# Optimization experiments

Measured on AMD Instinct MI355X. Metric: run time of the kernel, lower is better.

The kernel has to match this reference:

```python
import jax, jax.numpy as jnp
import numpy as np

B, T, D = 2, 4096, 1024
H, HD = 16, 64
KV = H * HD  # 1024


def setup_inputs() -> dict:
    key = jax.random.key(0)
    ks = jax.random.split(key, 6)
    sc = lambda k, shape, s: jax.random.normal(k, shape, jnp.float32) * s
    return {
        "x": sc(ks[0], (B, T, D), 1.0),
        "W_in": sc(ks[1], (D, 4 * KV), D ** -0.5),      # in_proj (in, out) layout
        "W_ba": sc(ks[2], (D, 2 * H), D ** -0.5),       # ba_proj
        "conv_w": sc(ks[3], (3 * KV, 1, 4), 0.5),       # depthwise conv, (O, I/groups=1, K)
        "dt_bias": jnp.ones((H,), jnp.float32),
        "A_log": jnp.log(jax.random.uniform(ks[4], (H,), jnp.float32, 1e-3, 16.0)),
        "norm_w": jnp.ones((HD,), jnp.float32),
        "W_o": sc(ks[5], (KV, D), KV ** -0.5),
    }


def _l2norm(t, eps=1e-6):
    return t * jax.lax.rsqrt(jnp.sum(t * t, axis=-1, keepdims=True) + eps)


def reference(x, W_in, W_ba, conv_w, dt_bias, A_log, norm_w, W_o):
    Bb, Tt, _ = x.shape
    qkvz = x @ W_in                                  # [B,T,4*KV]
    q, k, v, z = jnp.split(qkvz, 4, axis=-1)
    b, a = jnp.split(x @ W_ba, 2, axis=-1)           # [B,T,H] each

    # causal depthwise conv (kernel 4, left pad 3) + SiLU on concat(q,k,v)
    qkv = jnp.concatenate([q, k, v], axis=-1).transpose(0, 2, 1)  # [B,3KV,T]
    qkv = jax.lax.conv_general_dilated(
        qkv, conv_w, window_strides=(1,), padding=[(3, 0)],
        feature_group_count=3 * KV, dimension_numbers=("NCH", "OIH", "NCH"))
    qkv = jax.nn.silu(qkv).transpose(0, 2, 1)        # [B,T,3KV]
    q, k, v = jnp.split(qkv, 3, axis=-1)

    rs = lambda t: t.reshape(Bb, Tt, H, HD)
    q, k, v, z = rs(q), rs(k), rs(v), rs(z)

    beta = jax.nn.sigmoid(b)                         # [B,T,H]
    A = jnp.exp(jnp.maximum(A_log, -2.3))            # [H]
    g = -A * jax.nn.softplus(a + dt_bias)            # [B,T,H], log decay <= 0

    # fla use_qk_l2norm_in_kernel=True: l2-normalize q,k; q scaled by d^-0.5
    q = _l2norm(q) * (HD ** -0.5)
    k = _l2norm(k)

    # gated delta rule recurrence over time (state S: [B,H,dk,dv])
    tm = lambda t: jnp.swapaxes(t, 0, 1)             # time-major

    def step(S, inp):
        qt, kt, vt, gt, bt = inp
        S = S * jnp.exp(gt)[..., None, None]
        pred = jnp.einsum("bhk,bhkv->bhv", kt, S)
        S = S + jnp.einsum("bhk,bhv->bhkv", kt, (vt - pred) * bt[..., None])
        o = jnp.einsum("bhk,bhkv->bhv", qt, S)
        return S, o

    S0 = jnp.zeros((Bb, H, HD, HD), jnp.float32)
    _, y = jax.lax.scan(step, S0, (tm(q), tm(k), tm(v), tm(g), tm(beta)))
    y = jnp.swapaxes(y, 0, 1)                        # [B,T,H,HD]

    # RMSNormGated over head_dim, gated by silu(z)
    y = y * jax.lax.rsqrt(jnp.mean(y * y, axis=-1, keepdims=True) + 1e-6)
    y = (norm_w * y) * jax.nn.silu(z)

    return y.reshape(Bb, Tt, KV) @ W_o
```

## Files before the change

kernel.cpp:

```cpp
#include <hip/hip_runtime.h>

typedef unsigned short u16;
typedef unsigned int u32;
typedef __attribute__((ext_vector_type(8))) __bf16 bf16x8;
typedef __attribute__((ext_vector_type(8))) _Float16 f16x8;
typedef __attribute__((ext_vector_type(4))) _Float16 f16x4;
typedef __attribute__((ext_vector_type(4))) float f32x4;

#define DEV __device__ __forceinline__

DEV u16 f2bf(float f) {
  u32 u = __float_as_uint(f);
  u += 0x7FFFu + ((u >> 16) & 1u);
  return (u16)(u >> 16);
}
DEV float bf2f(u16 h) { return __uint_as_float(((u32)h) << 16); }
DEV void splitbf(float f, u16& hi, u16& lo) {
  u16 h = f2bf(f);
  hi = h;
  lo = f2bf(f - bf2f(h));
}
DEV void split4(float4 v, ushort4& hh, ushort4& ll) {
  splitbf(v.x, hh.x, ll.x);
  splitbf(v.y, hh.y, ll.y);
  splitbf(v.z, hh.z, ll.z);
  splitbf(v.w, hh.w, ll.w);
}
DEV int SW(int r, int c) { return r * 64 + ((c) ^ ((r & 7) << 3)); }

DEV int SWG(int r, int c) {
  int db = ((r & 1) << 2) | ((c >> 3) & 3);
  int dbp = db ^ ((r >> 1) & 7);
  return ((r >> 1) << 6) | (dbp << 3) | (c & 7);
}
DEV size_t gidx_swz(size_t row, int col, int rowlen) {
  int rr7 = (int)((row >> 1) & 7);
  int db = (int)(((row & 1) << 2) | ((col >> 3) & 3));
  int dbp = db ^ rr7;
  size_t rowp = (row & ~(size_t)1) | (size_t)(dbp >> 2);
  int colp = (col & ~31) | ((dbp & 3) << 3) | (col & 7);
  return rowp * (size_t)rowlen + colp;
}

#define MFMA16(a,b,c) __builtin_amdgcn_mfma_f32_16x16x32_bf16((a),(b),(c),0,0,0)
#define MFMAH(a,b,c)  __builtin_amdgcn_mfma_f32_16x16x32_f16((a),(b),(c),0,0,0)
#define GLDS16(g,l) __builtin_amdgcn_global_load_lds((__attribute__((address_space(1))) void*)(g), (__attribute__((address_space(3))) void*)(l), 16, 0, 0)

DEV f32x4 mm3(bf16x8 ah, bf16x8 al, bf16x8 bh, bf16x8 bl, f32x4 acc) {
  acc = MFMA16(ah, bl, acc);
  acc = MFMA16(al, bh, acc);
  acc = MFMA16(ah, bh, acc);
  return acc;
}

__global__ __launch_bounds__(256) void k_cast_h(const float* __restrict__ in, _Float16* __restrict__ out, int n) {
  int idx = (blockIdx.x * 256 + threadIdx.x) * 4;
  if (idx + 3 < n) {
    float4 v = *(const float4*)(in + idx);
    f16x4 o = {(_Float16)v.x, (_Float16)v.y, (_Float16)v.z, (_Float16)v.w};
    const size_t row = (size_t)(idx >> 10);
    const int col = idx & 1023;
    *(f16x4*)(out + gidx_swz(row, col, 1024)) = o;
  }
}

__global__ __launch_bounds__(256) void k_transpose_h(const float* __restrict__ in, _Float16* __restrict__ out, int R, int Cc) {
  __shared__ float tile[64][65];
  int c0 = blockIdx.x * 64, r0 = blockIdx.y * 64;
  int lr = threadIdx.x >> 6, lc = threadIdx.x & 63;
#pragma unroll
  for (int i = 0; i < 16; ++i) {
    int r = lr + i * 4;
    tile[r][lc] = in[(size_t)(r0 + r) * Cc + c0 + lc];
  }
  __syncthreads();
#pragma unroll
  for (int i = 0; i < 16; ++i) {
    int oc = lr + i * 4;
    out[gidx_swz((size_t)(c0 + oc), r0 + lc, R)] = (_Float16)tile[lc][oc];
  }
}

__global__ __launch_bounds__(256) void k_transpose(const float* __restrict__ in, u16* __restrict__ out, int R, int Cc) {
  __shared__ float tile[64][65];
  int c0 = blockIdx.x * 64, r0 = blockIdx.y * 64;
  int lr = threadIdx.x >> 6, lc = threadIdx.x & 63;
#pragma unroll
  for (int i = 0; i < 16; ++i) {
    int r = lr + i * 4;
    tile[r][lc] = in[(size_t)(r0 + r) * Cc + c0 + lc];
  }
  __syncthreads();
#pragma unroll
  for (int i = 0; i < 16; ++i) {
    int oc = lr + i * 4;
    out[gidx_swz((size_t)(c0 + oc), r0 + lc, R)] = f2bf(tile[lc][oc]);
  }
}

__global__ __launch_bounds__(512, 2) void k_gemm_h(const _Float16* __restrict__ A, const _Float16* __restrict__ Bt,
                                                   u16* __restrict__ Cq, u16* __restrict__ Cz, int M, int N, int K) {
  __shared__ __align__(16) u16 As[2][256 * 32];
  __shared__ __align__(16) u16 Bs[2][256 * 32];
  const int tid = threadIdx.x;
  const int nwg = gridDim.x * gridDim.y;
  int bid = blockIdx.y * gridDim.x + blockIdx.x;
  bid = (bid & 7) * (nwg >> 3) + (bid >> 3);
  const int m0 = (bid / gridDim.x) * 256, n0 = (bid % gridDim.x) * 256;
  const int w = tid >> 6, l = tid & 63;
  const int wr = (w >> 1) * 64, wc = (w & 1) * 128;
  const int lrow = l & 15, lk = (l >> 4) * 8, rbase = (l >> 4) * 4;

  f32x4 acc[4][8];
#pragma unroll
  for (int i = 0; i < 4; ++i)
#pragma unroll
    for (int j = 0; j < 8; ++j) acc[i][j] = {0.f, 0.f, 0.f, 0.f};

  const _Float16* aBase = A + (size_t)m0 * K;
  const _Float16* bBase = Bt + (size_t)n0 * K;
  const int srow0 = tid >> 2, scol0 = (tid & 3) * 8;
  const int srow1 = (tid + 512) >> 2;

  auto STAGE = [&](int buf, int k0) {
    GLDS16(aBase + (size_t)srow0 * K + k0 + scol0, &As[buf][tid * 8]);
    GLDS16(aBase + (size_t)srow1 * K + k0 + scol0, &As[buf][4096 + tid * 8]);
    GLDS16(bBase + (size_t)srow0 * K + k0 + scol0, &Bs[buf][tid * 8]);
    GLDS16(bBase + (size_t)srow1 * K + k0 + scol0, &Bs[buf][4096 + tid * 8]);
  };

  STAGE(0, 0);
  __syncthreads();
  int cur = 0;
  for (int k0 = 0; k0 < K; k0 += 32) {
    if (k0 + 32 < K) STAGE(cur ^ 1, k0 + 32);
    f16x8 af[4], bfr[8];
#pragma unroll
    for (int i = 0; i < 4; ++i) af[i] = *(const f16x8*)&As[cur][SWG(wr + i * 16 + lrow, lk)];
#pragma unroll
    for (int j = 0; j < 8; ++j) bfr[j] = *(const f16x8*)&Bs[cur][SWG(wc + j * 16 + lrow, lk)];
#pragma unroll
    for (int i = 0; i < 4; ++i)
#pragma unroll
      for (int j = 0; j < 8; ++j) acc[i][j] = MFMAH(af[i], bfr[j], acc[i][j]);
    __syncthreads();
    cur ^= 1;
  }
#pragma unroll
  for (int i = 0; i < 4; ++i)
#pragma unroll
    for (int j = 0; j < 8; ++j)
#pragma unroll
      for (int r = 0; r < 4; ++r) {
        int row = m0 + wr + i * 16 + rbase + r;
        int col = n0 + wc + j * 16 + lrow;
        if (col < 3072) Cq[(size_t)row * 3072 + col] = f2bf(acc[i][j][r]);
        else            Cz[(size_t)row * 1024 + col - 3072] = f2bf(acc[i][j][r]);
      }
}

__global__ __launch_bounds__(256, 2) void k_gemm2(const u16* __restrict__ Ah, const u16* __restrict__ Al,
                                               const u16* __restrict__ Bt, float* __restrict__ Cf,
                                               int M, int N, int K) {
  __shared__ __align__(16) u16 Ash[2][128 * 32];
  __shared__ __align__(16) u16 Asl[2][128 * 32];
  __shared__ __align__(16) u16 Bs[2][128 * 32];
  const int tid = threadIdx.x;
  const int nwg = gridDim.x * gridDim.y;
  int bid = blockIdx.y * gridDim.x + blockIdx.x;
  bid = (bid & 7) * (nwg >> 3) + (bid >> 3);
  const int m0 = (bid / gridDim.x) * 128, n0 = (bid % gridDim.x) * 128;
  const int w = tid >> 6, l = tid & 63;
  const int wr = (w >> 1) * 64, wc = (w & 1) * 64;
  const int lrow = l & 15, lk = (l >> 4) * 8, rbase = (l >> 4) * 4;
  const int srow = tid >> 2, scol = (tid & 3) * 8;

  f32x4 acc[4][4];
#pragma unroll
  for (int i = 0; i < 4; ++i)
#pragma unroll
    for (int j = 0; j < 4; ++j) acc[i][j] = {0.f, 0.f, 0.f, 0.f};

  const u16* ahBase = Ah + (size_t)m0 * K;
  const u16* alBase = Al + (size_t)m0 * K;
  const u16* bBase  = Bt + (size_t)n0 * K;

  auto STAGE = [&](int buf, int k0) {
    GLDS16(ahBase + (size_t)srow * K + k0 + scol,        &Ash[buf][tid * 8]);
    GLDS16(ahBase + (size_t)(srow + 64) * K + k0 + scol, &Ash[buf][2048 + tid * 8]);
    GLDS16(alBase + (size_t)srow * K + k0 + scol,        &Asl[buf][tid * 8]);
    GLDS16(alBase + (size_t)(srow + 64) * K + k0 + scol, &Asl[buf][2048 + tid * 8]);
    GLDS16(bBase + (size_t)srow * K + k0 + scol,         &Bs[buf][tid * 8]);
    GLDS16(bBase + (size_t)(srow + 64) * K + k0 + scol,  &Bs[buf][2048 + tid * 8]);
  };

  STAGE(0, 0);
  __syncthreads();
  int cur = 0;
  for (int k0 = 0; k0 < K; k0 += 32) {
    if (k0 + 32 < K) STAGE(cur ^ 1, k0 + 32);
    bf16x8 afh[4], afl[4], bfr[4];
#pragma unroll
    for (int i = 0; i < 4; ++i) afh[i] = *(const bf16x8*)&Ash[cur][SWG(wr + i * 16 + lrow, lk)];
#pragma unroll
    for (int i = 0; i < 4; ++i) afl[i] = *(const bf16x8*)&Asl[cur][SWG(wr + i * 16 + lrow, lk)];
#pragma unroll
    for (int j = 0; j < 4; ++j) bfr[j] = *(const bf16x8*)&Bs[cur][SWG(wc + j * 16 + lrow, lk)];
#pragma unroll
    for (int i = 0; i < 4; ++i)
#pragma unroll
      for (int j = 0; j < 4; ++j) {
        acc[i][j] = MFMA16(afl[i], bfr[j], acc[i][j]);
        acc[i][j] = MFMA16(afh[i], bfr[j], acc[i][j]);
      }
    __syncthreads();
    cur ^= 1;
  }
#pragma unroll
  for (int i = 0; i < 4; ++i)
#pragma unroll
    for (int j = 0; j < 4; ++j)
#pragma unroll
      for (int r = 0; r < 4; ++r) {
        int row = m0 + wr + i * 16 + rbase + r;
        int col = n0 + wc + j * 16 + lrow;
        Cf[(size_t)row * N + col] = acc[i][j][r];
      }
}

__global__ __launch_bounds__(256) void k_ba(const float* __restrict__ x, const float* __restrict__ Wba,
                                            const float* __restrict__ dt_bias, const float* __restrict__ A_log,
                                            float* __restrict__ betaO, float* __restrict__ gO) {
  __shared__ float xs[4][1024];
  const int wid = threadIdx.x >> 6, lane = threadIdx.x & 63;
  const int m = blockIdx.x * 4 + wid;
#pragma unroll
  for (int i = 0; i < 16; ++i) xs[wid][lane + 64 * i] = x[(size_t)m * 1024 + lane + 64 * i];
  __syncthreads();
  const int n = lane & 31, half = lane >> 5;
  float acc = 0.f;
  const float* wp = Wba + n;
  const int kk0 = half * 512;
#pragma unroll 8
  for (int kk = kk0; kk < kk0 + 512; ++kk) acc += xs[wid][kk] * wp[kk * 32];
  acc += __shfl_xor(acc, 32);
  if (lane < 32) {
    if (n < 16) {
      betaO[(size_t)m * 16 + n] = 1.f / (1.f + expf(-acc));
    } else {
      int h = n - 16;
      float xx = acc + dt_bias[h];
      float sp = (xx > 20.f) ? xx : log1pf(expf(xx));
      gO[(size_t)m * 16 + h] = -expf(fmaxf(A_log[h], -2.3f)) * sp;
    }
  }
}

__global__ __launch_bounds__(256) void k_conv(const u16* __restrict__ qkv3, const float* __restrict__ convw,
                                              u16* __restrict__ qhG, u16* __restrict__ qlG,
                                              u16* __restrict__ khG, u16* __restrict__ klG,
                                              u16* __restrict__ vhG, u16* __restrict__ vlG) {
  __shared__ float cs[3072];
  __shared__ float innorm[32];
  const int bt = blockIdx.x;
  const int bb = bt >> 12, tt = bt & 4095;
  const int tid = threadIdx.x;
  const size_t rb = (size_t)bb * 4096;
#pragma unroll
  for (int s = 0; s < 3; ++s) {
    const int c4 = tid * 4 + s * 1024;
    float cwa[4][4];
#pragma unroll
    for (int e = 0; e < 4; ++e) {
      float4 t = *(const float4*)&convw[(c4 + e) * 4];
      cwa[e][0] = t.x; cwa[e][1] = t.y; cwa[e][2] = t.z; cwa[e][3] = t.w;
    }
    float acc[4] = {0.f, 0.f, 0.f, 0.f};
#pragma unroll
    for (int j = 0; j < 4; ++j) {
      const int tau = tt - 3 + j;
      if (tau >= 0) {
        ushort4 kv = *(const ushort4*)&qkv3[(rb + tau) * 3072 + c4];
        acc[0] += bf2f(kv.x) * cwa[0][j];
        acc[1] += bf2f(kv.y) * cwa[1][j];
        acc[2] += bf2f(kv.z) * cwa[2][j];
        acc[3] += bf2f(kv.w) * cwa[3][j];
      }
    }
#pragma unroll
    for (int e = 0; e < 4; ++e) cs[c4 + e] = acc[e] / (1.f + expf(-acc[e]));
  }
  __syncthreads();
  {
    const int grp = tid >> 3, off = (tid & 7) * 8;
    const float* p = cs + grp * 64 + off;
    float s = 0.f;
#pragma unroll
    for (int i = 0; i < 8; ++i) s += p[i] * p[i];
    s += __shfl_xor(s, 1); s += __shfl_xor(s, 2); s += __shfl_xor(s, 4);
    if ((tid & 7) == 0) innorm[grp] = rsqrtf(s + 1e-6f);
  }
  __syncthreads();
  const int h = tid >> 4, d4 = (tid & 15) * 4;
  const size_t ob = ((size_t)(bb * 16 + h) * 64 + (tt >> 6)) * 4096 + SW(tt & 63, d4);
  {
    const int ci = h * 64 + d4;
    const float sc = innorm[h] * 0.125f;
    float4 o = {cs[ci] * sc, cs[ci + 1] * sc, cs[ci + 2] * sc, cs[ci + 3] * sc};
    ushort4 hh, ll;
    split4(o, hh, ll);
    *(ushort4*)&qhG[ob] = hh;
    *(ushort4*)&qlG[ob] = ll;
  }
  {
    const int ci = 1024 + h * 64 + d4;
    const float sc = innorm[16 + h];
    float4 o = {cs[ci] * sc, cs[ci + 1] * sc, cs[ci + 2] * sc, cs[ci + 3] * sc};
    ushort4 hh, ll;
    split4(o, hh, ll);
    *(ushort4*)&khG[ob] = hh;
    *(ushort4*)&klG[ob] = ll;
  }
  {
    const int ci = 2048 + h * 64 + d4;
    float4 o = {cs[ci], cs[ci + 1], cs[ci + 2], cs[ci + 3]};
    ushort4 hh, ll;
    split4(o, hh, ll);
    *(ushort4*)&vhG[ob] = hh;
    *(ushort4*)&vlG[ob] = ll;
  }
}

__global__ __launch_bounds__(64) void k_prep(const u16* __restrict__ khG, const u16* __restrict__ klG,
                                             const float* __restrict__ gG, const float* __restrict__ betaG,
                                             float* __restrict__ gcG, u16* __restrict__ Tgh, u16* __restrict__ Tgl) {
  __shared__ __align__(16) char pmem[16384];
  u16* Kbh = (u16*)pmem;
  u16* Kbl = (u16*)(pmem + 8192);
  float* Af = (float*)pmem;
  __shared__ float gcs[64], bs[64];
  const int bhc = blockIdx.x;
  const int c = bhc & 63, h = (bhc >> 6) & 15, bb = bhc >> 10;
  const int lane = threadIdx.x;
  const int t0 = c * 64;
  const size_t rowbase = (size_t)bb * 4096;
  const size_t ktile = (size_t)bhc * 4096;
#pragma unroll
  for (int i = 0; i < 8; ++i) {
    const int idx = lane + 64 * i;
    GLDS16(khG + ktile + idx * 8, &Kbh[idx * 8]);
    GLDS16(klG + ktile + idx * 8, &Kbl[idx * 8]);
  }
  {
    float gv = gG[(rowbase + t0 + lane) * 16 + h];
    float sc = gv;
#pragma unroll
    for (int off = 1; off < 64; off <<= 1) {
      float o = __shfl_up(sc, off);
      if (lane >= off) sc += o;
    }
    gcs[lane] = sc;
    bs[lane] = betaG[(rowbase + t0 + lane) * 16 + h];
    gcG[(size_t)bhc * 64 + lane] = sc;
  }
  __syncthreads();
  const int lrow = lane & 15, lk8 = (lane >> 4) * 8, rbase = (lane >> 4) * 4;
  f32x4 acc[4][4];
#pragma unroll
  for (int i = 0; i < 4; ++i)
#pragma unroll
    for (int j = 0; j < 4; ++j) acc[i][j] = {0.f, 0.f, 0.f, 0.f};
#pragma unroll
  for (int ks = 0; ks < 2; ++ks) {
    bf16x8 afh[4], afl[4], bfh[4], bfl[4];
#pragma unroll
    for (int i = 0; i < 4; ++i) {
      afh[i] = *(const bf16x8*)&Kbh[SW(i * 16 + lrow, ks * 32 + lk8)];
      afl[i] = *(const bf16x8*)&Kbl[SW(i * 16 + lrow, ks * 32 + lk8)];
    }
#pragma unroll
    for (int j = 0; j < 4; ++j) {
      bfh[j] = *(const bf16x8*)&Kbh[SW(j * 16 + lrow, ks * 32 + lk8)];
      bfl[j] = *(const bf16x8*)&Kbl[SW(j * 16 + lrow, ks * 32 + lk8)];
    }
#pragma unroll
    for (int i = 0; i < 4; ++i)
#pragma unroll
      for (int j = 0; j < 4; ++j) acc[i][j] = mm3(afh[i], afl[i], bfh[j], bfl[j], acc[i][j]);
  }
  __syncthreads();
#pragma unroll
  for (int i = 0; i < 4; ++i)
#pragma unroll
    for (int j = 0; j < 4; ++j)
#pragma unroll
      for (int r = 0; r < 4; ++r) {
        int t = i * 16 + rbase + r, s = j * 16 + lrow;
        Af[t * 64 + s] = (s < t) ? bs[t] * expf(gcs[t] - gcs[s]) * acc[i][j][r] : 0.f;
      }
  __syncthreads();
  float x[64];
#pragma unroll
  for (int t = 0; t < 64; ++t) {
    float sum = 0.f;
#pragma unroll
    for (int s4 = 0; s4 + 4 <= t; s4 += 4) {
      float4 a4 = *(const float4*)&Af[t * 64 + s4];
      sum += a4.x * x[s4] + a4.y * x[s4 + 1] + a4.z * x[s4 + 2] + a4.w * x[s4 + 3];
    }
#pragma unroll
    for (int s = (t & ~3); s < t; ++s) sum += Af[t * 64 + s] * x[s];
    x[t] = ((t == lane) ? 1.f : 0.f) - sum;
  }
#pragma unroll
  for (int t = 0; t < 64; ++t) {
    u16 hi, lo;
    splitbf(x[t], hi, lo);
    Tgh[(size_t)bhc * 4096 + SW(t, lane)] = hi;
    Tgl[(size_t)bhc * 4096 + SW(t, lane)] = lo;
  }
}

__global__ __launch_bounds__(256) void k_mn(const u16* __restrict__ khG, const u16* __restrict__ klG,
                                            const u16* __restrict__ vhG, const u16* __restrict__ vlG,
                                            const u16* __restrict__ Tgh, const u16* __restrict__ Tgl,
                                            const float* __restrict__ gcG, const float* __restrict__ betaG,
                                            u16* __restrict__ Mh, u16* __restrict__ Ml,
                                            u16* __restrict__ Nh, u16* __restrict__ Nl) {
  extern __shared__ __align__(16) char smem[];
  u16* base = (u16*)smem;
  u16* Tbh  = base + 0 * 4096;
  u16* Tbl  = base + 1 * 4096;
  u16* X1h  = base + 2 * 4096;
  u16* X1l  = base + 3 * 4096;
  u16* KdTh = base + 4 * 4096;
  u16* KdTl = base + 5 * 4096;
  u16* X2h  = base + 6 * 4096;
  u16* X2l  = base + 7 * 4096;
  float* gcs = (float*)(base + 8 * 4096);
  float* bs  = gcs + 64;

  const int bhc = blockIdx.x;
  const int c = bhc & 63, h = (bhc >> 6) & 15, bb = bhc >> 10;
  const int tid = threadIdx.x, w = tid >> 6, l = tid & 63;
  const int lrow = l & 15, lk8 = (l >> 4) * 8, rbase = (l >> 4) * 4;
  const int t0 = c * 64;
  const size_t rowbase = (size_t)bb * 4096;
  const size_t ktile = (size_t)bhc * 4096;

  if (tid < 64) {
    gcs[tid] = gcG[(size_t)bhc * 64 + tid];
    bs[tid] = betaG[(rowbase + t0 + tid) * 16 + h];
  }
#pragma unroll
  for (int i = 0; i < 2; ++i) {
    const int idx = tid + 256 * i;
    const int off = idx * 8;
    *(float4*)&Tbh[off] = *(const float4*)&Tgh[(size_t)bhc * 4096 + off];
    *(float4*)&Tbl[off] = *(const float4*)&Tgl[(size_t)bhc * 4096 + off];
  }
  __syncthreads();
  const float gc63 = gcs[63];
#pragma unroll
  for (int i = 0; i < 16; ++i) {
    const int flat = tid + 256 * i;
    const int s = flat >> 6, d = flat & 63;
    const int sws = SW(s, d);
    const float kf = bf2f(khG[ktile + sws]) + bf2f(klG[ktile + sws]);
    const float gv = gcs[s], bv = bs[s];
    u16 hh, ll;
    splitbf(bv * expf(gv) * kf, hh, ll);
    X1h[SW(d, s)] = hh; X1l[SW(d, s)] = ll;
    splitbf(expf(gc63 - gv) * kf, hh, ll);
    KdTh[SW(d, s)] = hh; KdTl[SW(d, s)] = ll;
    const float vv = bf2f(vhG[ktile + sws]) + bf2f(vlG[ktile + sws]);
    splitbf(bv * vv, hh, ll);
    X2h[SW(d, s)] = hh; X2l[SW(d, s)] = ll;
  }
  __syncthreads();

  f32x4 aW[4], aU[4];
#pragma unroll
  for (int j = 0; j < 4; ++j) { aW[j] = {0.f,0.f,0.f,0.f}; aU[j] = {0.f,0.f,0.f,0.f}; }
#pragma unroll
  for (int ks = 0; ks < 2; ++ks) {
    const int ao = SW(w * 16 + lrow, ks * 32 + lk8);
    bf16x8 aTh = *(const bf16x8*)&Tbh[ao];
    bf16x8 aTl = *(const bf16x8*)&Tbl[ao];
#pragma unroll
    for (int j = 0; j < 4; ++j) {
      const int bo = SW(j * 16 + lrow, ks * 32 + lk8);
      aW[j] = mm3(aTh, aTl, *(const bf16x8*)&X1h[bo], *(const bf16x8*)&X1l[bo], aW[j]);
      aU[j] = mm3(aTh, aTl, *(const bf16x8*)&X2h[bo], *(const bf16x8*)&X2l[bo], aU[j]);
    }
  }
  __syncthreads();
#pragma unroll
  for (int j = 0; j < 4; ++j)
#pragma unroll
    for (int r = 0; r < 4; ++r) {
      const int t = w * 16 + rbase + r, dcol = j * 16 + lrow;
      u16 hh, ll;
      splitbf(aW[j][r], hh, ll);
      X1h[SW(dcol, t)] = hh; X1l[SW(dcol, t)] = ll;
      splitbf(aU[j][r], hh, ll);
      X2h[SW(dcol, t)] = hh; X2l[SW(dcol, t)] = ll;
    }
  __syncthreads();

  f32x4 aM[4], aN[4];
#pragma unroll
  for (int j = 0; j < 4; ++j) { aM[j] = {0.f,0.f,0.f,0.f}; aN[j] = {0.f,0.f,0.f,0.f}; }
#pragma unroll
  for (int ks = 0; ks < 2; ++ks) {
    const int ao = SW(w * 16 + lrow, ks * 32 + lk8);
    bf16x8 aKh = *(const bf16x8*)&KdTh[ao];
    bf16x8 aKl = *(const bf16x8*)&KdTl[ao];
#pragma unroll
    for (int j = 0; j < 4; ++j) {
      const int bo = SW(j * 16 + lrow, ks * 32 + lk8);
      aM[j] = mm3(aKh, aKl, *(const bf16x8*)&X1h[bo], *(const bf16x8*)&X1l[bo], aM[j]);
      aN[j] = mm3(aKh, aKl, *(const bf16x8*)&X2h[bo], *(const bf16x8*)&X2l[bo], aN[j]);
    }
  }
  __syncthreads();
  const float decC = expf(gc63);
#pragma unroll
  for (int j = 0; j < 4; ++j)
#pragma unroll
    for (int r = 0; r < 4; ++r) {
      const int d = w * 16 + rbase + r, d2 = j * 16 + lrow;
      u16 hh, ll;
      splitbf(((d == d2) ? decC : 0.f) - aM[j][r], hh, ll);
      X1h[SW(d, d2)] = hh; X1l[SW(d, d2)] = ll;
      splitbf(aN[j][r], hh, ll);
      X2h[SW(d, d2)] = hh; X2l[SW(d, d2)] = ll;
    }
  __syncthreads();
#pragma unroll
  for (int i = 0; i < 2; ++i) {
    const int idx = tid + 256 * i;
    const int off = idx * 8;
    *(float4*)&Mh[(size_t)bhc * 4096 + off] = *(const float4*)&X1h[off];
    *(float4*)&Ml[(size_t)bhc * 4096 + off] = *(const float4*)&X1l[off];
    *(float4*)&Nh[(size_t)bhc * 4096 + off] = *(const float4*)&X2h[off];
    *(float4*)&Nl[(size_t)bhc * 4096 + off] = *(const float4*)&X2l[off];
  }
}

__global__ __launch_bounds__(256) void k_seg(const u16* __restrict__ Mh, const u16* __restrict__ Ml,
                                             const u16* __restrict__ Nh, const u16* __restrict__ Nl,
                                             u16* __restrict__ Msegh, u16* __restrict__ Msegl,
                                             u16* __restrict__ Nsegh, u16* __restrict__ Nsegl) {
  extern __shared__ __align__(16) char smem[];
  u16* base = (u16*)smem;
  u16* MaTh = base + 0 * 4096;
  u16* MaTl = base + 1 * 4096;
  u16* NaTh = base + 2 * 4096;
  u16* NaTl = base + 3 * 4096;
  u16* sMh  = base + 4 * 4096;
  u16* sMl  = base + 5 * 4096;
  u16* sNh  = base + 6 * 4096;
  u16* sNl  = base + 7 * 4096;

  const int blk = blockIdx.x;
  const size_t cbase = (size_t)(blk >> 3) * 64 + (blk & 7) * 8;
  const int tid = threadIdx.x, w = tid >> 6, l = tid & 63;
  const int lrow = l & 15, lk8 = (l >> 4) * 8, rbase = (l >> 4) * 4;

#pragma unroll
  for (int i = 0; i < 2; ++i) {
    const int off = (tid + 256 * i) * 8;
    *(float4*)&sMh[off] = *(const float4*)&Mh[cbase * 4096 + off];
    *(float4*)&sMl[off] = *(const float4*)&Ml[cbase * 4096 + off];
    *(float4*)&sNh[off] = *(const float4*)&Nh[cbase * 4096 + off];
    *(float4*)&sNl[off] = *(const float4*)&Nl[cbase * 4096 + off];
  }
  __syncthreads();
#pragma unroll
  for (int i = 0; i < 16; ++i) {
    const int flat = tid + 256 * i;
    const int a = flat >> 6, b = flat & 63;
    MaTh[SW(a, b)] = sMh[SW(b, a)];
    MaTl[SW(a, b)] = sMl[SW(b, a)];
    NaTh[SW(a, b)] = sNh[SW(b, a)];
    NaTl[SW(a, b)] = sNl[SW(b, a)];
  }
  __syncthreads();

  for (int j = 1; j < 8; ++j) {
#pragma unroll
    for (int i = 0; i < 2; ++i) {
      const int off = (tid + 256 * i) * 8;
      *(float4*)&sMh[off] = *(const float4*)&Mh[(cbase + j) * 4096 + off];
      *(float4*)&sMl[off] = *(const float4*)&Ml[(cbase + j) * 4096 + off];
      *(float4*)&sNh[off] = *(const float4*)&Nh[(cbase + j) * 4096 + off];
      *(float4*)&sNl[off] = *(const float4*)&Nl[(cbase + j) * 4096 + off];
    }
    __syncthreads();
    f32x4 aM2[4], aN2[4];
#pragma unroll
    for (int jj = 0; jj < 4; ++jj) { aM2[jj] = {0.f,0.f,0.f,0.f}; aN2[jj] = {0.f,0.f,0.f,0.f}; }
#pragma unroll
    for (int ks = 0; ks < 2; ++ks) {
      const int ao = SW(w * 16 + lrow, ks * 32 + lk8);
      bf16x8 aCh = *(const bf16x8*)&sMh[ao];
      bf16x8 aCl = *(const bf16x8*)&sMl[ao];
#pragma unroll
      for (int jj = 0; jj < 4; ++jj) {
        const int bo = SW(jj * 16 + lrow, ks * 32 + lk8);
        aM2[jj] = mm3(aCh, aCl, *(const bf16x8*)&MaTh[bo], *(const bf16x8*)&MaTl[bo], aM2[jj]);
        aN2[jj] = mm3(aCh, aCl, *(const bf16x8*)&NaTh[bo], *(const bf16x8*)&NaTl[bo], aN2[jj]);
      }
    }
    __syncthreads();
#pragma unroll
    for (int jj = 0; jj < 4; ++jj)
#pragma unroll
      for (int r = 0; r < 4; ++r) {
        const int t = w * 16 + rbase + r, col = jj * 16 + lrow;
        u16 hh, ll;
        splitbf(aM2[jj][r], hh, ll);
        MaTh[SW(col, t)] = hh; MaTl[SW(col, t)] = ll;
        const float nv = aN2[jj][r] + bf2f(sNh[SW(t, col)]) + bf2f(sNl[SW(t, col)]);
        splitbf(nv, hh, ll);
        NaTh[SW(col, t)] = hh; NaTl[SW(col, t)] = ll;
      }
    __syncthreads();
  }
#pragma unroll
// ... 225 lines not shown
      for (int j = 0; j < 2; ++j) {
        const int bo = SW((jh * 2 + j) * 16 + lrow, ks * 32 + lk8);
        au[j] = mm3(aTh, aTl, *(const bf16x8*)&RTh[bo], *(const bf16x8*)&RTl[bo], au[j]);
      }
    }
#pragma unroll
    for (int j = 0; j < 2; ++j)
#pragma unroll
      for (int r = 0; r < 4; ++r) {
        u16 uh, ul;
        splitbf(au[j][r], uh, ul);
        const int o = SW((jh * 2 + j) * 16 + lrow, wrow * 16 + rbase + r);
        UTh[o] = uh;
        UTl[o] = ul;
      }
    __syncthreads();

    if (pf) {
      GLDS16(Tgh + (size_t)(bh * 64 + (c + 1)) * 4096 + o8, &Tbh[o8]);
      GLDS16(Tgl + (size_t)(bh * 64 + (c + 1)) * 4096 + o8, &Tbl[o8]);
    }

    f32x4 amu[2], as_[2];
#pragma unroll
    for (int j = 0; j < 2; ++j) { amu[j] = {0.f,0.f,0.f,0.f}; as_[j] = {0.f,0.f,0.f,0.f}; }
#pragma unroll
    for (int ks = 0; ks < 2; ++ks) {
      const int ao = SW(wrow * 16 + lrow, ks * 32 + lk8);
      bf16x8 aMh = *(const bf16x8*)&Mqh[ao];
      bf16x8 aMl = *(const bf16x8*)&Mql[ao];
      bf16x8 aKdh = *(const bf16x8*)&KdTh[ao];
      bf16x8 aKdl = *(const bf16x8*)&KdTl[ao];
#pragma unroll
      for (int j = 0; j < 2; ++j) {
        const int bo = SW((jh * 2 + j) * 16 + lrow, ks * 32 + lk8);
        bf16x8 bUh = *(const bf16x8*)&UTh[bo];
        bf16x8 bUl = *(const bf16x8*)&UTl[bo];
        amu[j] = mm3(aMh, aMl, bUh, bUl, amu[j]);
        as_[j] = mm3(aKdh, aKdl, bUh, bUl, as_[j]);
      }
    }
    float yv_[4][2];
#pragma unroll
    for (int r = 0; r < 4; ++r) {
      const int t = wrow * 16 + rbase + r;
      const float gt = etF[t];
      float ss = 0.f;
#pragma unroll
      for (int j = 0; j < 2; ++j) {
        yv_[r][j] = gt * aqs[j][r] + amu[j][r];
        ss += yv_[r][j] * yv_[r][j];
      }
      ss += __shfl_xor(ss, 1); ss += __shfl_xor(ss, 2); ss += __shfl_xor(ss, 4); ss += __shfl_xor(ss, 8);
      if (lrow == 0) ssP[jh * 64 + t] = ss;
    }
    __syncthreads();
#pragma unroll
    for (int r = 0; r < 4; ++r) {
      const int t = wrow * 16 + rbase + r;
      const float rstd = rsqrtf((ssP[t] + ssP[64 + t]) * (1.f / 64.f) + 1e-6f);
#pragma unroll
      for (int j = 0; j < 2; ++j) {
        const int col = (jh * 2 + j) * 16 + lrow;
        const float zz = bf2f(Zb[SW(t, col)]);
        const float yv = yv_[r][j] * rstd * nws[col] * (zz / (1.f + expf(-zz)));
        u16 yh, yl;
        splitbf(yv, yh, yl);
        Ybh[SW(t, col)] = yh;
        Ybl[SW(t, col)] = yl;
      }
    }
    {
      const float decC = etF[63];
#pragma unroll
      for (int j = 0; j < 2; ++j)
#pragma unroll
        for (int r = 0; r < 4; ++r) {
          const int d = wrow * 16 + rbase + r, col = (jh * 2 + j) * 16 + lrow;
          const int o = SW(col, d);
          const float s0 = bf2f(SbTh[o]) + bf2f(SbTl[o]);
          const float sv = decC * s0 + as_[j][r];
          u16 sh, sl;
          splitbf(sv, sh, sl);
          SbTh[o] = sh;
          SbTl[o] = sl;
        }
    }
    __syncthreads();

    {
      const size_t gsw = gidx_swz(rowbase + t0 + zr, h * 64 + zc8, 1024);
      *(float4*)&Yhi[gsw] = *(const float4*)&Ybh[SW(zr, zc8)];
      *(float4*)&Ylo[gsw] = *(const float4*)&Ybl[SW(zr, zc8)];
    }
    if (pf) {
      *(float4*)&Zb[SW(zr, zc8)] = pz;
      if (tid < 64) {
        float g63 = __shfl(pgc, 63);
        gcs[tid] = pgc; bs[tid] = pbs;
        esF[tid] = expf(g63 - pgc);
        etF[tid] = expf(pgc);
      }
    }
    __syncthreads();
  }
}

extern "C" void kernel_launch(void* const* d_in, const int* in_sizes, int n_in,
                              void* d_out, int out_size, void* d_ws, size_t ws_size,
                              hipStream_t stream) {
  (void)in_sizes; (void)n_in; (void)out_size; (void)ws_size;
  const float* x       = (const float*)d_in[0];
  const float* W_in    = (const float*)d_in[1];
  const float* W_ba    = (const float*)d_in[2];
  const float* conv_w  = (const float*)d_in[3];
  const float* dt_bias = (const float*)d_in[4];
  const float* A_log   = (const float*)d_in[5];
  const float* norm_w  = (const float*)d_in[6];
  const float* W_o     = (const float*)d_in[7];
  float* out = (float*)d_out;
  char* ws = (char*)d_ws;
  const size_t MB = 1048576;

  _Float16* xh = (_Float16*)(ws + 0);
  u16* MhB   = (u16*)(ws + 0);
  u16* YhiB  = (u16*)(ws + 0);
  u16* MlB   = (u16*)(ws + 16 * MB);
  u16* YloB  = (u16*)(ws + 16 * MB);
  _Float16* WinT = (_Float16*)(ws + 32 * MB);
  float* gB  = (float*)(ws + 32 * MB);
  float* bB  = (float*)(ws + 32 * MB + 524288);
  float* gcB = (float*)(ws + 33 * MB);
  u16* Ssegh = (u16*)(ws + 34 * MB);
  u16* Ssegl = (u16*)(ws + 36 * MB);
  u16* Msegh = (u16*)(ws + 38 * MB);
  u16* Msegl = (u16*)(ws + 40 * MB);
  u16* Nsegh = (u16*)(ws + 42 * MB);
  u16* Nsegl = (u16*)(ws + 44 * MB);
  u16* WoT   = (u16*)(ws + 48 * MB);
  u16* qkv3  = (u16*)(ws + 50 * MB);
  u16* NhB   = (u16*)(ws + 50 * MB);
  u16* NlB   = (u16*)(ws + 66 * MB);
  u16* zbB   = (u16*)(ws + 98 * MB);
  u16* qhG   = (u16*)(ws + 114 * MB);
  u16* qlG   = (u16*)(ws + 130 * MB);
  u16* khG   = (u16*)(ws + 146 * MB);
  u16* klG   = (u16*)(ws + 162 * MB);
  u16* vhG   = (u16*)(ws + 178 * MB);
  u16* vlG   = (u16*)(ws + 194 * MB);
  u16* TghB  = (u16*)(ws + 210 * MB);
  u16* TglB  = (u16*)(ws + 226 * MB);

  const int SCAN_LDS = 19 * 8192 + 448 * 4;
  const int MN_LDS   = 8 * 8192 + 512;
  const int SEG_LDS  = 8 * 8192;

  k_cast_h<<<8192, 256, 0, stream>>>(x, xh, 8388608);
  k_transpose_h<<<dim3(64, 16), 256, 0, stream>>>(W_in, WinT, 1024, 4096);
  k_transpose<<<dim3(16, 16), 256, 0, stream>>>(W_o, WoT, 1024, 1024);
  k_gemm_h<<<dim3(16, 32), 512, 0, stream>>>(xh, WinT, qkv3, zbB, 8192, 4096, 1024);
  k_ba<<<2048, 256, 0, stream>>>(x, W_ba, dt_bias, A_log, bB, gB);
  k_conv<<<8192, 256, 0, stream>>>(qkv3, conv_w, qhG, qlG, khG, klG, vhG, vlG);
  k_prep<<<2048, 64, 0, stream>>>(khG, klG, gB, bB, gcB, TghB, TglB);
  hipFuncSetAttribute((const void*)k_mn, hipFuncAttributeMaxDynamicSharedMemorySize, MN_LDS);
  k_mn<<<2048, 256, MN_LDS, stream>>>(khG, klG, vhG, vlG, TghB, TglB, gcB, bB, MhB, MlB, NhB, NlB);
  hipFuncSetAttribute((const void*)k_seg, hipFuncAttributeMaxDynamicSharedMemorySize, SEG_LDS);
  k_seg<<<256, 256, SEG_LDS, stream>>>(MhB, MlB, NhB, NlB, Msegh, Msegl, Nsegh, Nsegl);
  k_bound<<<32, 256, 0, stream>>>(Msegh, Msegl, Nsegh, Nsegl, Ssegh, Ssegl);
  hipFuncSetAttribute((const void*)k_scan2, hipFuncAttributeMaxDynamicSharedMemorySize, SCAN_LDS);
  k_scan2<<<256, 512, SCAN_LDS, stream>>>(qhG, qlG, khG, klG, vhG, vlG, zbB, TghB, TglB, gcB, bB, norm_w,
                                          Ssegh, Ssegl, YhiB, YloB);
  k_gemm2<<<dim3(8, 64), 256, 0, stream>>>(YhiB, YloB, WoT, out, 8192, 1024, 1024);
}
```

Baseline: 512.9 us.

## Fuse chunk prep into the M/N kernel and widen output GEMM tile

Merges k_prep (the K·Kᵀ Gram matrix, cumulative gate sums and the triangular-inverse T matrix) into the M/N kernel as k_prepmn. The Gram MFMAs are spread across four waves, and the other three waves build the KdT/X2 operands while wave 0 runs the serial triangular solve. This removes a launch and the round trip of T through global memory, but the triangular solve still runs on a single wave. Separately, the output projection GEMM tile grows from 128x128 to 128x256, giving more accumulators per thread and half as many workgroups. The trade is more register pressure and less occupancy in that GEMM.

```diff
diff --git a/kernel.cpp b/kernel.cpp
--- a/kernel.cpp
+++ b/kernel.cpp
@@ -164,34 +164,36 @@
                                                int M, int N, int K) {
   __shared__ __align__(16) u16 Ash[2][128 * 32];
   __shared__ __align__(16) u16 Asl[2][128 * 32];
-  __shared__ __align__(16) u16 Bs[2][128 * 32];
+  __shared__ __align__(16) u16 Bs[2][256 * 32];
   const int tid = threadIdx.x;
   const int nwg = gridDim.x * gridDim.y;
   int bid = blockIdx.y * gridDim.x + blockIdx.x;
   bid = (bid & 7) * (nwg >> 3) + (bid >> 3);
-  const int m0 = (bid / gridDim.x) * 128, n0 = (bid % gridDim.x) * 128;
+  const int m0 = (bid / gridDim.x) * 128, n0 = (bid % gridDim.x) * 256;
   const int w = tid >> 6, l = tid & 63;
-  const int wr = (w >> 1) * 64, wc = (w & 1) * 64;
+  const int wr = (w >> 1) * 64, wc = (w & 1) * 128;
   const int lrow = l & 15, lk = (l >> 4) * 8, rbase = (l >> 4) * 4;
   const int srow = tid >> 2, scol = (tid & 3) * 8;
 
-  f32x4 acc[4][4];
+  f32x4 acc[4][8];
 #pragma unroll
   for (int i = 0; i < 4; ++i)
 #pragma unroll
-    for (int j = 0; j < 4; ++j) acc[i][j] = {0.f, 0.f, 0.f, 0.f};
+    for (int j = 0; j < 8; ++j) acc[i][j] = {0.f, 0.f, 0.f, 0.f};
 
   const u16* ahBase = Ah + (size_t)m0 * K;
   const u16* alBase = Al + (size_t)m0 * K;
   const u16* bBase  = Bt + (size_t)n0 * K;
 
   auto STAGE = [&](int buf, int k0) {
-    GLDS16(ahBase + (size_t)srow * K + k0 + scol,        &Ash[buf][tid * 8]);
-    GLDS16(ahBase + (size_t)(srow + 64) * K + k0 + scol, &Ash[buf][2048 + tid * 8]);
-    GLDS16(alBase + (size_t)srow * K + k0 + scol,        &Asl[buf][tid * 8]);
-    GLDS16(alBase + (size_t)(srow + 64) * K + k0 + scol, &Asl[buf][2048 + tid * 8]);
-    GLDS16(bBase + (size_t)srow * K + k0 + scol,         &Bs[buf][tid * 8]);
-    GLDS16(bBase + (size_t)(srow + 64) * K + k0 + scol,  &Bs[buf][2048 + tid * 8]);
+    GLDS16(ahBase + (size_t)srow * K + k0 + scol,         &Ash[buf][tid * 8]);
+    GLDS16(ahBase + (size_t)(srow + 64) * K + k0 + scol,  &Ash[buf][2048 + tid * 8]);
+    GLDS16(alBase + (size_t)srow * K + k0 + scol,         &Asl[buf][tid * 8]);
+    GLDS16(alBase + (size_t)(srow + 64) * K + k0 + scol,  &Asl[buf][2048 + tid * 8]);
+    GLDS16(bBase + (size_t)srow * K + k0 + scol,          &Bs[buf][tid * 8]);
+    GLDS16(bBase + (size_t)(srow + 64) * K + k0 + scol,   &Bs[buf][2048 + tid * 8]);
+    GLDS16(bBase + (size_t)(srow + 128) * K + k0 + scol,  &Bs[buf][4096 + tid * 8]);
+    GLDS16(bBase + (size_t)(srow + 192) * K + k0 + scol,  &Bs[buf][6144 + tid * 8]);
   };
 
   STAGE(0, 0);
@@ -199,17 +201,17 @@
   int cur = 0;
   for (int k0 = 0; k0 < K; k0 += 32) {
     if (k0 + 32 < K) STAGE(cur ^ 1, k0 + 32);
-    bf16x8 afh[4], afl[4], bfr[4];
+    bf16x8 afh[4], afl[4], bfr[8];
 #pragma unroll
     for (int i = 0; i < 4; ++i) afh[i] = *(const bf16x8*)&Ash[cur][SWG(wr + i * 16 + lrow, lk)];
 #pragma unroll
     for (int i = 0; i < 4; ++i) afl[i] = *(const bf16x8*)&Asl[cur][SWG(wr + i * 16 + lrow, lk)];
 #pragma unroll
-    for (int j = 0; j < 4; ++j) bfr[j] = *(const bf16x8*)&Bs[cur][SWG(wc + j * 16 + lrow, lk)];
+    for (int j = 0; j < 8; ++j) bfr[j] = *(const bf16x8*)&Bs[cur][SWG(wc + j * 16 + lrow, lk)];
 #pragma unroll
     for (int i = 0; i < 4; ++i)
 #pragma unroll
-      for (int j = 0; j < 4; ++j) {
+      for (int j = 0; j < 8; ++j) {
         acc[i][j] = MFMA16(afl[i], bfr[j], acc[i][j]);
         acc[i][j] = MFMA16(afh[i], bfr[j], acc[i][j]);
       }
@@ -219,7 +221,7 @@
 #pragma unroll
   for (int i = 0; i < 4; ++i)
 #pragma unroll
-    for (int j = 0; j < 4; ++j)
+    for (int j = 0; j < 8; ++j)
 #pragma unroll
       for (int r = 0; r < 4; ++r) {
         int row = m0 + wr + i * 16 + rbase + r;
@@ -331,112 +333,26 @@
   }
 }
 
-__global__ __launch_bounds__(64) void k_prep(const u16* __restrict__ khG, const u16* __restrict__ klG,
-                                             const float* __restrict__ gG, const float* __restrict__ betaG,
-                                             float* __restrict__ gcG, u16* __restrict__ Tgh, u16* __restrict__ Tgl) {
-  __shared__ __align__(16) char pmem[16384];
-  u16* Kbh = (u16*)pmem;
-  u16* Kbl = (u16*)(pmem + 8192);
-  float* Af = (float*)pmem;
-  __shared__ float gcs[64], bs[64];
-  const int bhc = blockIdx.x;
-  const int c = bhc & 63, h = (bhc >> 6) & 15, bb = bhc >> 10;
-  const int lane = threadIdx.x;
-  const int t0 = c * 64;
-  const size_t rowbase = (size_t)bb * 4096;
-  const size_t ktile = (size_t)bhc * 4096;
-#pragma unroll
-  for (int i = 0; i < 8; ++i) {
-    const int idx = lane + 64 * i;
-    GLDS16(khG + ktile + idx * 8, &Kbh[idx * 8]);
-    GLDS16(klG + ktile + idx * 8, &Kbl[idx * 8]);
-  }
-  {
-    float gv = gG[(rowbase + t0 + lane) * 16 + h];
-    float sc = gv;
-#pragma unroll
-    for (int off = 1; off < 64; off <<= 1) {
-      float o = __shfl_up(sc, off);
-      if (lane >= off) sc += o;
-    }
-    gcs[lane] = sc;
-    bs[lane] = betaG[(rowbase + t0 + lane) * 16 + h];
-    gcG[(size_t)bhc * 64 + lane] = sc;
-  }
-  __syncthreads();
-  const int lrow = lane & 15, lk8 = (lane >> 4) * 8, rbase = (lane >> 4) * 4;
-  f32x4 acc[4][4];
-#pragma unroll
-  for (int i = 0; i < 4; ++i)
-#pragma unroll
-    for (int j = 0; j < 4; ++j) acc[i][j] = {0.f, 0.f, 0.f, 0.f};
-#pragma unroll
-  for (int ks = 0; ks < 2; ++ks) {
-    bf16x8 afh[4], afl[4], bfh[4], bfl[4];
-#pragma unroll
-    for (int i = 0; i < 4; ++i) {
-      afh[i] = *(const bf16x8*)&Kbh[SW(i * 16 + lrow, ks * 32 + lk8)];
-      afl[i] = *(const bf16x8*)&Kbl[SW(i * 16 + lrow, ks * 32 + lk8)];
-    }
-#pragma unroll
-    for (int j = 0; j < 4; ++j) {
-      bfh[j] = *(const bf16x8*)&Kbh[SW(j * 16 + lrow, ks * 32 + lk8)];
-      bfl[j] = *(const bf16x8*)&Kbl[SW(j * 16 + lrow, ks * 32 + lk8)];
-    }
-#pragma unroll
-    for (int i = 0; i < 4; ++i)
-#pragma unroll
-      for (int j = 0; j < 4; ++j) acc[i][j] = mm3(afh[i], afl[i], bfh[j], bfl[j], acc[i][j]);
-  }
-  __syncthreads();
-#pragma unroll
-  for (int i = 0; i < 4; ++i)
-#pragma unroll
-    for (int j = 0; j < 4; ++j)
-#pragma unroll
-      for (int r = 0; r < 4; ++r) {
-        int t = i * 16 + rbase + r, s = j * 16 + lrow;
-        Af[t * 64 + s] = (s < t) ? bs[t] * expf(gcs[t] - gcs[s]) * acc[i][j][r] : 0.f;
-      }
-  __syncthreads();
-  float x[64];
-#pragma unroll
-  for (int t = 0; t < 64; ++t) {
-    float sum = 0.f;
-#pragma unroll
-    for (int s4 = 0; s4 + 4 <= t; s4 += 4) {
-      float4 a4 = *(const float4*)&Af[t * 64 + s4];
-      sum += a4.x * x[s4] + a4.y * x[s4 + 1] + a4.z * x[s4 + 2] + a4.w * x[s4 + 3];
-    }
-#pragma unroll
-    for (int s = (t & ~3); s < t; ++s) sum += Af[t * 64 + s] * x[s];
-    x[t] = ((t == lane) ? 1.f : 0.f) - sum;
-  }
-#pragma unroll
-  for (int t = 0; t < 64; ++t) {
-    u16 hi, lo;
-    splitbf(x[t], hi, lo);
-    Tgh[(size_t)bhc * 4096 + SW(t, lane)] = hi;
-    Tgl[(size_t)bhc * 4096 + SW(t, lane)] = lo;
-  }
-}
-
-__global__ __launch_bounds__(256) void k_mn(const u16* __restrict__ khG, const u16* __restrict__ klG,
-                                            const u16* __restrict__ vhG, const u16* __restrict__ vlG,
-                                            const u16* __restrict__ Tgh, const u16* __restrict__ Tgl,
-                                            const float* __restrict__ gcG, const float* __restrict__ betaG,
-                                            u16* __restrict__ Mh, u16* __restrict__ Ml,
-                                            u16* __restrict__ Nh, u16* __restrict__ Nl) {
+__global__ __launch_bounds__(256) void k_prepmn(const u16* __restrict__ khG, const u16* __restrict__ klG,
+                                                const u16* __restrict__ vhG, const u16* __restrict__ vlG,
+                                                const float* __restrict__ gG, const float* __restrict__ betaG,
+                                                float* __restrict__ gcG,
+                                                u16* __restrict__ Tgh, u16* __restrict__ Tgl,
+                                                u16* __restrict__ Mh, u16* __restrict__ Ml,
+                                                u16* __restrict__ Nh, u16* __restrict__ Nl) {
   extern __shared__ __align__(16) char smem[];
   u16* base = (u16*)smem;
-  u16* Tbh  = base + 0 * 4096;
-  u16* Tbl  = base + 1 * 4096;
+  u16* Kbh  = base + 0 * 4096;
+  u16* Kbl  = base + 1 * 4096;
+  u16* Tbh  = Kbh;
+  u16* Tbl  = Kbl;
   u16* X1h  = base + 2 * 4096;
   u16* X1l  = base + 3 * 4096;
   u16* KdTh = base + 4 * 4096;
   u16* KdTl = base + 5 * 4096;
   u16* X2h  = base + 6 * 4096;
   u16* X2l  = base + 7 * 4096;
+  float* Af = (float*)(base + 2 * 4096);
   float* gcs = (float*)(base + 8 * 4096);
   float* bs  = gcs + 64;
 
@@ -448,34 +364,98 @@
   const size_t rowbase = (size_t)bb * 4096;
   const size_t ktile = (size_t)bhc * 4096;
 
+#pragma unroll
+  for (int i = 0; i < 2; ++i) {
+    const int o8 = (tid + 256 * i) * 8;
+    GLDS16(khG + ktile + o8, &Kbh[o8]);
+    GLDS16(klG + ktile + o8, &Kbl[o8]);
+  }
   if (tid < 64) {
-    gcs[tid] = gcG[(size_t)bhc * 64 + tid];
+    float gv = gG[(rowbase + t0 + tid) * 16 + h];
+    float sc = gv;
+#pragma unroll
+    for (int off = 1; off < 64; off <<= 1) {
+      float o = __shfl_up(sc, off);
+      if (tid >= off) sc += o;
+    }
+    gcs[tid] = sc;
     bs[tid] = betaG[(rowbase + t0 + tid) * 16 + h];
-  }
-#pragma unroll
-  for (int i = 0; i < 2; ++i) {
-    const int idx = tid + 256 * i;
-    const int off = idx * 8;
-    *(float4*)&Tbh[off] = *(const float4*)&Tgh[(size_t)bhc * 4096 + off];
-    *(float4*)&Tbl[off] = *(const float4*)&Tgl[(size_t)bhc * 4096 + off];
-  }
-  __syncthreads();
+    gcG[(size_t)bhc * 64 + tid] = sc;
+  }
+  __syncthreads();
+
+  f32x4 acc[4];
+#pragma unroll
+  for (int j = 0; j < 4; ++j) acc[j] = {0.f, 0.f, 0.f, 0.f};
+#pragma unroll
+  for (int ks = 0; ks < 2; ++ks) {
+    bf16x8 afh = *(const bf16x8*)&Kbh[SW(w * 16 + lrow, ks * 32 + lk8)];
+    bf16x8 afl = *(const bf16x8*)&Kbl[SW(w * 16 + lrow, ks * 32 + lk8)];
+#pragma unroll
+    for (int j = 0; j < 4; ++j) {
+      bf16x8 bfh = *(const bf16x8*)&Kbh[SW(j * 16 + lrow, ks * 32 + lk8)];
+      bf16x8 bfl = *(const bf16x8*)&Kbl[SW(j * 16 + lrow, ks * 32 + lk8)];
+      acc[j] = mm3(afh, afl, bfh, bfl, acc[j]);
+    }
+  }
+  __syncthreads();
+#pragma unroll
+  for (int j = 0; j < 4; ++j)
+#pragma unroll
+    for (int r = 0; r < 4; ++r) {
+      const int t = w * 16 + rbase + r, s = j * 16 + lrow;
+      Af[t * 64 + s] = (s < t) ? bs[t] * expf(gcs[t] - gcs[s]) * acc[j][r] : 0.f;
+    }
+  __syncthreads();
+
   const float gc63 = gcs[63];
+  if (tid < 64) {
+    float x[64];
+#pragma unroll
+    for (int t = 0; t < 64; ++t) {
+      float sum = 0.f;
+#pragma unroll
+      for (int s4 = 0; s4 + 4 <= t; s4 += 4) {
+        float4 a4 = *(const float4*)&Af[t * 64 + s4];
+        sum += a4.x * x[s4] + a4.y * x[s4 + 1] + a4.z * x[s4 + 2] + a4.w * x[s4 + 3];
+      }
+#pragma unroll
+      for (int s = (t & ~3); s < t; ++s) sum += Af[t * 64 + s] * x[s];
+      x[t] = ((t == tid) ? 1.f : 0.f) - sum;
+    }
+#pragma unroll
+    for (int t = 0; t < 64; ++t) {
+      u16 hi, lo;
+      splitbf(x[t], hi, lo);
+      Tbh[SW(t, tid)] = hi;
+      Tbl[SW(t, tid)] = lo;
+      Tgh[(size_t)bhc * 4096 + SW(t, tid)] = hi;
+      Tgl[(size_t)bhc * 4096 + SW(t, tid)] = lo;
+    }
+  } else {
+    for (int i2 = tid - 64; i2 < 4096; i2 += 192) {
+      const int s = i2 >> 6, d = i2 & 63;
+      const int sws = SW(s, d);
+      const float kf = bf2f(khG[ktile + sws]) + bf2f(klG[ktile + sws]);
+      u16 hh, ll;
+      splitbf(expf(gc63 - gcs[s]) * kf, hh, ll);
+      KdTh[SW(d, s)] = hh; KdTl[SW(d, s)] = ll;
+      const float vv = bf2f(vhG[ktile + sws]) + bf2f(vlG[ktile + sws]);
+      splitbf(bs[s] * vv, hh, ll);
+      X2h[SW(d, s)] = hh; X2l[SW(d, s)] = ll;
+    }
+  }
+  __syncthreads();
+
 #pragma unroll
   for (int i = 0; i < 16; ++i) {
     const int flat = tid + 256 * i;
     const int s = flat >> 6, d = flat & 63;
     const int sws = SW(s, d);
     const float kf = bf2f(khG[ktile + sws]) + bf2f(klG[ktile + sws]);
-    const float gv = gcs[s], bv = bs[s];
     u16 hh, ll;
-    splitbf(bv * expf(gv) * kf, hh, ll);
+    splitbf(bs[s] * expf(gcs[s]) * kf, hh, ll);
     X1h[SW(d, s)] = hh; X1l[SW(d, s)] = ll;
-    splitbf(expf(gc63 - gv) * kf, hh, ll);
-    KdTh[SW(d, s)] = hh; KdTl[SW(d, s)] = ll;
-    const float vv = bf2f(vhG[ktile + sws]) + bf2f(vlG[ktile + sws]);
-    splitbf(bv * vv, hh, ll);
-    X2h[SW(d, s)] = hh; X2l[SW(d, s)] = ll;
   }
   __syncthreads();
 
@@ -1007,7 +987,7 @@
   u16* TglB  = (u16*)(ws + 226 * MB);
 
   const int SCAN_LDS = 19 * 8192 + 448 * 4;
-  const int MN_LDS   = 8 * 8192 + 512;
+  const int PMN_LDS  = 8 * 8192 + 512;
   const int SEG_LDS  = 8 * 8192;
 
   k_cast_h<<<8192, 256, 0, stream>>>(x, xh, 8388608);
@@ -1016,14 +996,14 @@
   k_gemm_h<<<dim3(16, 32), 512, 0, stream>>>(xh, WinT, qkv3, zbB, 8192, 4096, 1024);
   k_ba<<<2048, 256, 0, stream>>>(x, W_ba, dt_bias, A_log, bB, gB);
   k_conv<<<8192, 256, 0, stream>>>(qkv3, conv_w, qhG, qlG, khG, klG, vhG, vlG);
-  k_prep<<<2048, 64, 0, stream>>>(khG, klG, gB, bB, gcB, TghB, TglB);
-  hipFuncSetAttribute((const void*)k_mn, hipFuncAttributeMaxDynamicSharedMemorySize, MN_LDS);
-  k_mn<<<2048, 256, MN_LDS, stream>>>(khG, klG, vhG, vlG, TghB, TglB, gcB, bB, MhB, MlB, NhB, NlB);
+  hipFuncSetAttribute((const void*)k_prepmn, hipFuncAttributeMaxDynamicSharedMemorySize, PMN_LDS);
+  k_prepmn<<<2048, 256, PMN_LDS, stream>>>(khG, klG, vhG, vlG, gB, bB, gcB, TghB, TglB,
+                                           MhB, MlB, NhB, NlB);
   hipFuncSetAttribute((const void*)k_seg, hipFuncAttributeMaxDynamicSharedMemorySize, SEG_LDS);
   k_seg<<<256, 256, SEG_LDS, stream>>>(MhB, MlB, NhB, NlB, Msegh, Msegl, Nsegh, Nsegl);
   k_bound<<<32, 256, 0, stream>>>(Msegh, Msegl, Nsegh, Nsegl, Ssegh, Ssegl);
   hipFuncSetAttribute((const void*)k_scan2, hipFuncAttributeMaxDynamicSharedMemorySize, SCAN_LDS);
   k_scan2<<<256, 512, SCAN_LDS, stream>>>(qhG, qlG, khG, klG, vhG, vlG, zbB, TghB, TglB, gcB, bB, norm_w,
                                           Ssegh, Ssegl, YhiB, YloB);
-  k_gemm2<<<dim3(8, 64), 256, 0, stream>>>(YhiB, YloB, WoT, out, 8192, 1024, 1024);
-}
+  k_gemm2<<<dim3(4, 64), 256, 0, stream>>>(YhiB, YloB, WoT, out, 8192, 1024, 1024);
+}
```

Measured after the change: 537.7 us. 4.8% more time.
